# Optimization experiments

Measured on AMD Instinct MI355X. Metric: run time of the kernel, lower is better.

The kernel has to match this reference:

```python
import jax, jax.numpy as jnp
import numpy as np

TEMPERATURE = 8.0  # sqrt(d_k), d_k = 64

def setup_inputs() -> dict:
    key = jax.random.key(0)
    kq, kk, kv = jax.random.split(key, 3)
    B, S, D = 16, 4096, 64
    Q = jax.random.normal(kq, (B, S, D), dtype=jnp.float32)
    K = jax.random.normal(kk, (B, S, D), dtype=jnp.float32)
    V = jax.random.normal(kv, (B, S, D), dtype=jnp.float32)
    return {"Q": Q, "K": K, "V": V}

def reference(Q, K, V):
    # scores: [B, S, S]
    scores = jnp.einsum('bqd,bkd->bqk', Q, K) / TEMPERATURE
    attn = jax.nn.softmax(scores, axis=-1)
    # dropout(p=0.1) is identity in eval mode; omitted for deterministic reference
    x = jnp.einsum('bqk,bkd->bqd', attn, V)  # [B, S, D]
    return (x, attn)
```

## Files before the change

### kernel.cpp

```cpp
#include <hip/hip_runtime.h>

#define S 4096
#define D 64
#define NB 16

typedef _Float16 half8 __attribute__((ext_vector_type(8)));
typedef _Float16 half4 __attribute__((ext_vector_type(4)));
typedef float f32x4 __attribute__((ext_vector_type(4)));

__global__ void cvt_qk(const float* __restrict__ Q, const float* __restrict__ K,
                       _Float16* __restrict__ Qh, _Float16* __restrict__ Kh, int n) {
  int i = blockIdx.x * blockDim.x + threadIdx.x;
  int stride = gridDim.x * blockDim.x;
  for (; i < n; i += stride) {
    Qh[i] = (_Float16)(Q[i] * 0.125f);
    Kh[i] = (_Float16)(K[i]);
  }
}

__global__ void cvt_vt(const float* __restrict__ V, _Float16* __restrict__ Vt) {
  __shared__ float tile[64][65];
  int b = blockIdx.x >> 6;
  int s0 = (blockIdx.x & 63) * 64;
  const float* vb = V + ((size_t)b * S) * D;
  for (int i = threadIdx.x; i < 64 * 64; i += 256) {
    int sl = i >> 6, d = i & 63;
    tile[sl][d] = vb[(size_t)(s0 + sl) * D + d];
  }
  __syncthreads();
  _Float16* vtb = Vt + ((size_t)b * D) * S;
  for (int i = threadIdx.x; i < 64 * 64; i += 256) {
    int dl = i >> 6, sl = i & 63;
    vtb[(size_t)dl * S + s0 + sl] = (_Float16)tile[sl][dl];
  }
}

__global__ __launch_bounds__(512, 2) void attn_fused(
    const _Float16* __restrict__ Qh, const _Float16* __restrict__ Kh,
    const _Float16* __restrict__ Vt, float* __restrict__ X, float* __restrict__ Aout) {
  const int tid = threadIdx.x;
  const int w = tid >> 6;
  const int l = tid & 63;
  const int l15 = l & 15;
  const int lq = l >> 4;
  const int r4 = lq * 4;
  const int bx = blockIdx.x;
  const int b = bx >> 8;
  const int m0 = (bx & 255) * 16;

  const _Float16* qb = Qh + ((size_t)b * S + m0) * D;
  const _Float16* kb = Kh + ((size_t)b * S) * D;
  const _Float16* vtb = Vt + ((size_t)b * D) * S;

  __shared__ float lred[8][16];
  __shared__ __align__(16) char ubuf[8][4224];

  half8 qf0 = *(const half8*)(qb + (size_t)l15 * D + lq * 8);
  half8 qf1 = *(const half8*)(qb + (size_t)l15 * D + 32 + lq * 8);

  const int nbase = w * 512;

  half4 pk[32];
  float vsum[4] = {0.f, 0.f, 0.f, 0.f};
#pragma unroll
  for (int f = 0; f < 32; ++f) {
    const _Float16* kp = kb + (size_t)(nbase + f * 16 + l15) * D + lq * 8;
    half8 kf0 = *(const half8*)(kp);
    half8 kf1 = *(const half8*)(kp + 32);
    f32x4 a = (f32x4){0.f, 0.f, 0.f, 0.f};
    a = __builtin_amdgcn_mfma_f32_16x16x32_f16(qf0, kf0, a, 0, 0, 0);
    a = __builtin_amdgcn_mfma_f32_16x16x32_f16(qf1, kf1, a, 0, 0, 0);
#pragma unroll
    for (int j = 0; j < 4; ++j) {
      float p = __expf(a[j]);
      vsum[j] += p;
      pk[f][j] = (_Float16)p;
    }
  }
#pragma unroll
  for (int off = 1; off < 16; off <<= 1)
#pragma unroll
    for (int j = 0; j < 4; ++j) vsum[j] += __shfl_xor(vsum[j], off, 64);
  if (l15 == 0) {
#pragma unroll
    for (int j = 0; j < 4; ++j) lred[w][r4 + j] = vsum[j];
  }
  __syncthreads();

  float rinvX[4], rinvS[4];
#pragma unroll
  for (int j = 0; j < 4; ++j) {
    float s = 0.f;
#pragma unroll
    for (int ww = 0; ww < 8; ++ww) s += lred[ww][r4 + j];
    rinvX[j] = 1.0f / s;
  }
#pragma unroll
  for (int i = 0; i < 4; ++i) {
    float s = 0.f;
#pragma unroll
    for (int ww = 0; ww < 8; ++ww) s += lred[ww][lq + 4 * i];
    rinvS[i] = 1.0f / s;
  }

  _Float16(*st)[72] = (_Float16(*)[72])(ubuf[w]);
  float* arow = Aout + ((size_t)b * S + m0) * S + nbase;
  f32x4 xacc[4];
#pragma unroll
  for (int fd = 0; fd < 4; ++fd) xacc[fd] = (f32x4){0.f, 0.f, 0.f, 0.f};

#pragma unroll
  for (int c = 0; c < 8; ++c) {
#pragma unroll
    for (int ff = 0; ff < 4; ++ff)
#pragma unroll
      for (int j = 0; j < 4; ++j)
        st[r4 + j][ff * 16 + l15] = pk[c * 4 + ff][j];
    asm volatile("" ::: "memory");
#pragma unroll
    for (int i = 0; i < 4; ++i) {
      int r = lq + i * 4;
      half4 t = *(const half4*)&st[r][l15 * 4];
      f32x4 o;
#pragma unroll
      for (int q = 0; q < 4; ++q) o[q] = (float)t[q] * rinvS[i];
      *(f32x4*)(arow + (size_t)r * S + c * 64 + l15 * 4) = o;
    }
#pragma unroll
    for (int kh = 0; kh < 2; ++kh) {
      half8 af = *(const half8*)&st[l15][kh * 32 + lq * 8];
#pragma unroll
      for (int fd = 0; fd < 4; ++fd) {
        half8 bf = *(const half8*)(vtb + (size_t)(fd * 16 + l15) * S +
                                   nbase + c * 64 + kh * 32 + lq * 8);
        xacc[fd] = __builtin_amdgcn_mfma_f32_16x16x32_f16(af, bf, xacc[fd], 0, 0, 0);
      }
    }
    asm volatile("" ::: "memory");
  }

  asm volatile("" ::: "memory");
  float (*xr)[66] = (float(*)[66])(ubuf[w]);
#pragma unroll
  for (int fd = 0; fd < 4; ++fd)
#pragma unroll
    for (int j = 0; j < 4; ++j)
      xr[r4 + j][fd * 16 + l15] = xacc[fd][j] * rinvX[j];
  __syncthreads();
  float* xrow = X + ((size_t)b * S + m0) * D;
#pragma unroll
  for (int o = tid; o < 16 * 64; o += 512) {
    int r = o >> 6, d = o & 63;
    float s = 0.f;
#pragma unroll
    for (int ww = 0; ww < 8; ++ww) s += ((const float(*)[66])(ubuf[ww]))[r][d];
    xrow[(size_t)r * D + d] = s;
  }
}

extern "C" void kernel_launch(void* const* d_in, const int* in_sizes, int n_in,
                              void* d_out, int out_size, void* d_ws, size_t ws_size,
                              hipStream_t stream) {
  const float* Q = (const float*)d_in[0];
  const float* K = (const float*)d_in[1];
  const float* V = (const float*)d_in[2];
  float* X = (float*)d_out;
  float* A = X + (size_t)NB * S * D;
  _Float16* Qh = (_Float16*)d_ws;
  _Float16* Kh = Qh + (size_t)NB * S * D;
  _Float16* Vt = Kh + (size_t)NB * S * D;
  int n = NB * S * D;
  cvt_qk<<<2048, 256, 0, stream>>>(Q, K, Qh, Kh, n);
  cvt_vt<<<NB * 64, 256, 0, stream>>>(V, Vt);
  attn_fused<<<NB * 256, 512, 0, stream>>>(Qh, Kh, Vt, X, A);
}
```

Baseline: 758.1 us.

## Split fused attention into PV pass and recomputing attention-store pass

```diff
diff --git a/kernel.cpp b/kernel.cpp
--- a/kernel.cpp
+++ b/kernel.cpp
@@ -35,9 +35,9 @@
   }
 }
 
-__global__ __launch_bounds__(512, 2) void attn_fused(
+__global__ __launch_bounds__(512, 2) void attn_pv(
     const _Float16* __restrict__ Qh, const _Float16* __restrict__ Kh,
-    const _Float16* __restrict__ Vt, float* __restrict__ X, float* __restrict__ Aout) {
+    const _Float16* __restrict__ Vt, float* __restrict__ X, float* __restrict__ Lsum) {
   const int tid = threadIdx.x;
   const int w = tid >> 6;
   const int l = tid & 63;
@@ -59,52 +59,9 @@
   half8 qf1 = *(const half8*)(qb + (size_t)l15 * D + 32 + lq * 8);
 
   const int nbase = w * 512;
-
-  half4 pk[32];
+  _Float16(*st)[72] = (_Float16(*)[72])(ubuf[w]);
+
   float vsum[4] = {0.f, 0.f, 0.f, 0.f};
-#pragma unroll
-  for (int f = 0; f < 32; ++f) {
-    const _Float16* kp = kb + (size_t)(nbase + f * 16 + l15) * D + lq * 8;
-    half8 kf0 = *(const half8*)(kp);
-    half8 kf1 = *(const half8*)(kp + 32);
-    f32x4 a = (f32x4){0.f, 0.f, 0.f, 0.f};
-    a = __builtin_amdgcn_mfma_f32_16x16x32_f16(qf0, kf0, a, 0, 0, 0);
-    a = __builtin_amdgcn_mfma_f32_16x16x32_f16(qf1, kf1, a, 0, 0, 0);
-#pragma unroll
-    for (int j = 0; j < 4; ++j) {
-      float p = __expf(a[j]);
-      vsum[j] += p;
-      pk[f][j] = (_Float16)p;
-    }
-  }
-#pragma unroll
-  for (int off = 1; off < 16; off <<= 1)
-#pragma unroll
-    for (int j = 0; j < 4; ++j) vsum[j] += __shfl_xor(vsum[j], off, 64);
-  if (l15 == 0) {
-#pragma unroll
-    for (int j = 0; j < 4; ++j) lred[w][r4 + j] = vsum[j];
-  }
-  __syncthreads();
-
-  float rinvX[4], rinvS[4];
-#pragma unroll
-  for (int j = 0; j < 4; ++j) {
-    float s = 0.f;
-#pragma unroll
-    for (int ww = 0; ww < 8; ++ww) s += lred[ww][r4 + j];
-    rinvX[j] = 1.0f / s;
-  }
-#pragma unroll
-  for (int i = 0; i < 4; ++i) {
-    float s = 0.f;
-#pragma unroll
-    for (int ww = 0; ww < 8; ++ww) s += lred[ww][lq + 4 * i];
-    rinvS[i] = 1.0f / s;
-  }
-
-  _Float16(*st)[72] = (_Float16(*)[72])(ubuf[w]);
-  float* arow = Aout + ((size_t)b * S + m0) * S + nbase;
   f32x4 xacc[4];
 #pragma unroll
   for (int fd = 0; fd < 4; ++fd) xacc[fd] = (f32x4){0.f, 0.f, 0.f, 0.f};
@@ -112,20 +69,21 @@
 #pragma unroll
   for (int c = 0; c < 8; ++c) {
 #pragma unroll
-    for (int ff = 0; ff < 4; ++ff)
-#pragma unroll
-      for (int j = 0; j < 4; ++j)
-        st[r4 + j][ff * 16 + l15] = pk[c * 4 + ff][j];
-    asm volatile("" ::: "memory");
-#pragma unroll
-    for (int i = 0; i < 4; ++i) {
-      int r = lq + i * 4;
-      half4 t = *(const half4*)&st[r][l15 * 4];
-      f32x4 o;
-#pragma unroll
-      for (int q = 0; q < 4; ++q) o[q] = (float)t[q] * rinvS[i];
-      *(f32x4*)(arow + (size_t)r * S + c * 64 + l15 * 4) = o;
-    }
+    for (int ff = 0; ff < 4; ++ff) {
+      const _Float16* kp = kb + (size_t)(nbase + (c * 4 + ff) * 16 + l15) * D + lq * 8;
+      half8 kf0 = *(const half8*)(kp);
+      half8 kf1 = *(const half8*)(kp + 32);
+      f32x4 a = (f32x4){0.f, 0.f, 0.f, 0.f};
+      a = __builtin_amdgcn_mfma_f32_16x16x32_f16(qf0, kf0, a, 0, 0, 0);
+      a = __builtin_amdgcn_mfma_f32_16x16x32_f16(qf1, kf1, a, 0, 0, 0);
+#pragma unroll
+      for (int j = 0; j < 4; ++j) {
+        float p = __expf(a[j]);
+        vsum[j] += p;
+        st[r4 + j][ff * 16 + l15] = (_Float16)p;
+      }
+    }
+    asm volatile("" ::: "memory");
 #pragma unroll
     for (int kh = 0; kh < 2; ++kh) {
       half8 af = *(const half8*)&st[l15][kh * 32 + lq * 8];
@@ -139,7 +97,32 @@
     asm volatile("" ::: "memory");
   }
 
-  asm volatile("" ::: "memory");
+#pragma unroll
+  for (int off = 1; off < 16; off <<= 1)
+#pragma unroll
+    for (int j = 0; j < 4; ++j) vsum[j] += __shfl_xor(vsum[j], off, 64);
+  if (l15 == 0) {
+#pragma unroll
+    for (int j = 0; j < 4; ++j) lred[w][r4 + j] = vsum[j];
+  }
+  __syncthreads();
+
+  if (tid < 16) {
+    float s = 0.f;
+#pragma unroll
+    for (int ww = 0; ww < 8; ++ww) s += lred[ww][tid];
+    Lsum[(size_t)b * S + m0 + tid] = __logf(s);
+  }
+
+  float rinvX[4];
+#pragma unroll
+  for (int j = 0; j < 4; ++j) {
+    float s = 0.f;
+#pragma unroll
+    for (int ww = 0; ww < 8; ++ww) s += lred[ww][r4 + j];
+    rinvX[j] = 1.0f / s;
+  }
+
   float (*xr)[66] = (float(*)[66])(ubuf[w]);
 #pragma unroll
   for (int fd = 0; fd < 4; ++fd)
@@ -155,6 +138,63 @@
 #pragma unroll
     for (int ww = 0; ww < 8; ++ww) s += ((const float(*)[66])(ubuf[ww]))[r][d];
     xrow[(size_t)r * D + d] = s;
+  }
+}
+
+__global__ __launch_bounds__(512, 4) void attn_store(
+    const _Float16* __restrict__ Qh, const _Float16* __restrict__ Kh,
+    const float* __restrict__ Lsum, float* __restrict__ Aout) {
+  const int tid = threadIdx.x;
+  const int w = tid >> 6;
+  const int l = tid & 63;
+  const int l15 = l & 15;
+  const int lq = l >> 4;
+  const int r4 = lq * 4;
+  const int bx = blockIdx.x;
+  const int b = bx >> 8;
+  const int m0 = (bx & 255) * 16;
+
+  const _Float16* qb = Qh + ((size_t)b * S + m0) * D;
+  const _Float16* kb = Kh + ((size_t)b * S) * D;
+
+  __shared__ __align__(16) _Float16 stg[8][16][72];
+
+  half8 qf0 = *(const half8*)(qb + (size_t)l15 * D + lq * 8);
+  half8 qf1 = *(const half8*)(qb + (size_t)l15 * D + 32 + lq * 8);
+
+  float ls[4];
+#pragma unroll
+  for (int j = 0; j < 4; ++j) ls[j] = Lsum[(size_t)b * S + m0 + r4 + j];
+
+  const int nbase = w * 512;
+  _Float16(*st)[72] = stg[w];
+  float* arow = Aout + ((size_t)b * S + m0) * S + nbase;
+
+#pragma unroll
+  for (int c = 0; c < 8; ++c) {
+#pragma unroll
+    for (int ff = 0; ff < 4; ++ff) {
+      const _Float16* kp = kb + (size_t)(nbase + (c * 4 + ff) * 16 + l15) * D + lq * 8;
+      half8 kf0 = *(const half8*)(kp);
+      half8 kf1 = *(const half8*)(kp + 32);
+      f32x4 a = (f32x4){0.f, 0.f, 0.f, 0.f};
+      a = __builtin_amdgcn_mfma_f32_16x16x32_f16(qf0, kf0, a, 0, 0, 0);
+      a = __builtin_amdgcn_mfma_f32_16x16x32_f16(qf1, kf1, a, 0, 0, 0);
+#pragma unroll
+      for (int j = 0; j < 4; ++j)
+        st[r4 + j][ff * 16 + l15] = (_Float16)__expf(a[j] - ls[j]);
+    }
+    asm volatile("" ::: "memory");
+#pragma unroll
+    for (int i = 0; i < 4; ++i) {
+      int r = lq + i * 4;
+      half4 t = *(const half4*)&st[r][l15 * 4];
+      f32x4 o;
+#pragma unroll
+      for (int q = 0; q < 4; ++q) o[q] = (float)t[q];
+      *(f32x4*)(arow + (size_t)r * S + c * 64 + l15 * 4) = o;
+    }
+    asm volatile("" ::: "memory");
   }
 }
 
@@ -169,8 +209,10 @@
   _Float16* Qh = (_Float16*)d_ws;
   _Float16* Kh = Qh + (size_t)NB * S * D;
   _Float16* Vt = Kh + (size_t)NB * S * D;
+  float* Lsum = (float*)(Vt + (size_t)NB * S * D);
   int n = NB * S * D;
   cvt_qk<<<2048, 256, 0, stream>>>(Q, K, Qh, Kh, n);
   cvt_vt<<<NB * 64, 256, 0, stream>>>(V, Vt);
-  attn_fused<<<NB * 256, 512, 0, stream>>>(Qh, Kh, Vt, X, A);
-}
+  attn_pv<<<NB * 256, 512, 0, stream>>>(Qh, Kh, Vt, X, Lsum);
+  attn_store<<<NB * 256, 512, 0, stream>>>(Qh, Kh, Lsum, A);
+}
```

Result: slower. 857.4 us (+13.1%).
